# Kernel optimization log

Hardware: AMD Instinct MI355X
Metric: run time of the kernel (lower is better)

The kernel has to match this reference:

```python
import jax, jax.numpy as jnp
import numpy as np

DK = 128
B, S = 16, 2048

def setup_inputs() -> dict:
    key = jax.random.key(0)
    kq, kk, kv = jax.random.split(key, 3)
    q = jax.random.normal(kq, (B, S, DK), dtype=jnp.float32)
    k = jax.random.normal(kk, (B, S, DK), dtype=jnp.float32)
    v = jax.random.normal(kv, (B, S, DK), dtype=jnp.float32)
    return {"q": q, "k": k, "v": v}

def reference(q, k, v):
    # scores: [B, S, S]
    scale = 1.0 / jnp.sqrt(jnp.float32(DK))
    scores = jnp.einsum("bqd,bkd->bqk", q, k) * scale
    probs = jax.nn.softmax(scores, axis=-1)
    # dropout is identity in eval mode (training=None)
    return jnp.einsum("bqk,bkd->bqd", probs, v)
```

## Files before the change

kernel.cpp:

```cpp
#include <hip/hip_runtime.h>
#include <hip/hip_bf16.h>

#define BATCH 16
#define SEQ   2048
#define DK    128
#define NT    (SEQ / 64)
#define SC2   0.12751744f
#define THRAW 90.5f

typedef __attribute__((ext_vector_type(8))) short short8v;
typedef __attribute__((ext_vector_type(4))) float float4v;

typedef const __attribute__((address_space(1))) unsigned int* gas_t;
typedef __attribute__((address_space(3))) unsigned int* las_t;

__device__ inline void gl_lds16(const void* g, void* l) {
    __builtin_amdgcn_global_load_lds((gas_t)g, (las_t)l, 16, 0, 0);
}

__device__ inline short f2bf(float f) {
    __hip_bfloat16 h = __float2bfloat16(f);
    unsigned short u;
    __builtin_memcpy(&u, &h, sizeof(u));
    return (short)u;
}

__device__ inline unsigned cvt_pk_bf16(float a, float b) {
    unsigned r;
    asm("v_cvt_pk_bf16_f32 %0, %1, %2" : "=v"(r) : "v"(a), "v"(b));
    return r;
}

__global__ __launch_bounds__(256)
void conv_k_kernel(const float* __restrict__ k, short* __restrict__ kb)
{
    size_t i = ((size_t)blockIdx.x * 256 + threadIdx.x) * 8;
    float4 a = *reinterpret_cast<const float4*>(k + i);
    float4 b = *reinterpret_cast<const float4*>(k + i + 4);
    short8v t;
    t[0] = f2bf(a.x); t[1] = f2bf(a.y); t[2] = f2bf(a.z); t[3] = f2bf(a.w);
    t[4] = f2bf(b.x); t[5] = f2bf(b.y); t[6] = f2bf(b.z); t[7] = f2bf(b.w);
    *reinterpret_cast<short8v*>(kb + i) = t;
}

__global__ __launch_bounds__(256)
void transpose_v_kernel(const float* __restrict__ v, short* __restrict__ vt)
{
    __shared__ float tile[32][33];
    const int tx = threadIdx.x & 31;
    const int ty = threadIdx.x >> 5;
    const int b  = blockIdx.z;
    const int s0 = blockIdx.x * 32;
    const int d0 = blockIdx.y * 32;

    const float* vb = v + ((size_t)b * SEQ + s0) * DK + d0;
#pragma unroll
    for (int i = 0; i < 4; ++i) {
        int r = ty + 8 * i;
        tile[r][tx] = vb[(size_t)r * DK + tx];
    }
    __syncthreads();

    const int s   = s0 + tx;
    const int t   = s >> 6;
    const int kvl = s & 63;
    const int pos = ((kvl >> 5) << 5) | (((kvl >> 2) & 3) << 3) | (((kvl >> 4) & 1) << 2) | (kvl & 3);
    const size_t col = (size_t)(t << 6) + pos;

    short* vtb = vt + ((size_t)b * DK + d0) * SEQ;
#pragma unroll
    for (int i = 0; i < 4; ++i) {
        int r = ty + 8 * i;
        vtb[(size_t)r * SEQ + col] = f2bf(tile[tx][r]);
    }
}

__global__ __launch_bounds__(256)
void attn_fwd_v4(const float* __restrict__ q,
                 const short* __restrict__ kb,
                 const short* __restrict__ vt,
                 float* __restrict__ out)
{
    __shared__ __align__(16) char lds[65536];

    const int tid  = threadIdx.x;
    const int lane = tid & 63;
    const int wave = tid >> 6;
    const int b    = blockIdx.y;
    const int q0   = blockIdx.x * 64 + wave * 16;

    const int row = lane & 15;
    const int grp = lane >> 4;
    const int swz = (row & 7) << 4;

    const float* qb = q + ((size_t)b * SEQ + q0) * DK;
    short8v qf[4];
#pragma unroll
    for (int c = 0; c < 4; ++c) {
        const float* p = qb + row * DK + c * 32 + grp * 8;
        float4 x = *reinterpret_cast<const float4*>(p);
        float4 y = *reinterpret_cast<const float4*>(p + 4);
        union { unsigned u[4]; short8v v; } pk;
        pk.u[0] = cvt_pk_bf16(x.x, x.y);
        pk.u[1] = cvt_pk_bf16(x.z, x.w);
        pk.u[2] = cvt_pk_bf16(y.x, y.y);
        pk.u[3] = cvt_pk_bf16(y.z, y.w);
        qf[c] = pk.v;
    }

    const char* kB = (const char*)(kb + (size_t)b * SEQ * DK);
    const char* vB = (const char*)(vt + (size_t)b * DK * SEQ);

    const int kSrcCol = (lane & 15) << 4;
    const int vSrcCol = (lane & 7) << 4;

    float m_run = -1e30f;
    float l_run = 0.0f;
    float4v o[8];
#pragma unroll
    for (int i = 0; i < 8; ++i) { o[i][0] = 0.f; o[i][1] = 0.f; o[i][2] = 0.f; o[i][3] = 0.f; }

    auto STAGE = [&](int bufsel, int t) {
        char* Kd = lds + bufsel * 32768;
        char* Vd = Kd + 16384;
        const char* ksrc = kB + (size_t)t * 64 * 256;
        const char* vsrc = vB + (size_t)t * 128;
#pragma unroll
        for (int i = 0; i < 4; ++i) {
            const int c  = wave * 4 + i;
            const int kr = 4 * c + (lane >> 4);
            gl_lds16(ksrc + (size_t)kr * 256 + (kSrcCol ^ ((kr & 7) << 4)),
                     Kd + c * 1024);
            const int vd = 8 * c + (lane >> 3);
            gl_lds16(vsrc + (size_t)vd * 4096 + (vSrcCol ^ ((vd & 7) << 4)),
                     Vd + c * 1024);
        }
    };

    STAGE(0, 0);
    __syncthreads();

    int buf = 0;
    for (int t = 0; t < NT; ++t) {
        if (t + 1 < NT) STAGE(buf ^ 1, t + 1);

        const char* Kl = lds + buf * 32768;
        const char* Vl = Kl + 16384;

        float4v s[4];
        __builtin_amdgcn_s_setprio(1);
#pragma unroll
        for (int sub = 0; sub < 4; ++sub) {
            s[sub][0] = 0.f; s[sub][1] = 0.f; s[sub][2] = 0.f; s[sub][3] = 0.f;
            const char* kr = Kl + (sub * 16 + row) * 256;
#pragma unroll
            for (int c = 0; c < 4; ++c) {
                short8v kf = *reinterpret_cast<const short8v*>(kr + (((c << 6) | (grp << 4)) ^ swz));
                s[sub] = __builtin_amdgcn_mfma_f32_16x16x32_bf16(kf, qf[c], s[sub], 0, 0, 0);
            }
        }
        __builtin_amdgcn_s_setprio(0);

        float p[16];
#pragma unroll
        for (int sub = 0; sub < 4; ++sub)
#pragma unroll
            for (int r = 0; r < 4; ++r) p[sub * 4 + r] = s[sub][r];

        float mx = p[0];
#pragma unroll
        for (int i = 1; i < 16; ++i) mx = fmaxf(mx, p[i]);
        mx = fmaxf(mx, __shfl_xor(mx, 16));
        mx = fmaxf(mx, __shfl_xor(mx, 32));

        if (!__all(mx <= m_run + THRAW)) {
            const float mnew  = fmaxf(m_run, mx);
            const float alpha = exp2f((m_run - mnew) * SC2);
            l_run *= alpha;
            m_run = mnew;
            float aq[4];
#pragma unroll
            for (int r = 0; r < 4; ++r) aq[r] = __shfl(alpha, grp * 4 + r);
#pragma unroll
            for (int dblk = 0; dblk < 8; ++dblk)
#pragma unroll
                for (int r = 0; r < 4; ++r) o[dblk][r] *= aq[r];
        }

        float tsum = 0.f;
#pragma unroll
        for (int i = 0; i < 16; ++i) { p[i] = exp2f((p[i] - m_run) * SC2); tsum += p[i]; }
        tsum += __shfl_xor(tsum, 16);
        tsum += __shfl_xor(tsum, 32);
        l_run += tsum;

        short8v pf[2];
#pragma unroll
        for (int p2 = 0; p2 < 2; ++p2) {
            union { unsigned u[4]; short8v v; } pk;
            pk.u[0] = cvt_pk_bf16(p[8 * p2 + 0], p[8 * p2 + 1]);
            pk.u[1] = cvt_pk_bf16(p[8 * p2 + 2], p[8 * p2 + 3]);
            pk.u[2] = cvt_pk_bf16(p[8 * p2 + 4], p[8 * p2 + 5]);
            pk.u[3] = cvt_pk_bf16(p[8 * p2 + 6], p[8 * p2 + 7]);
            pf[p2] = pk.v;
        }

        __builtin_amdgcn_s_setprio(1);
#pragma unroll
        for (int dblk = 0; dblk < 8; ++dblk) {
            const char* vr = Vl + (dblk * 16 + row) * 128;
#pragma unroll
            for (int p2 = 0; p2 < 2; ++p2) {
                short8v vf = *reinterpret_cast<const short8v*>(vr + ((((p2 << 2) | grp) << 4) ^ swz));
                o[dblk] = __builtin_amdgcn_mfma_f32_16x16x32_bf16(pf[p2], vf, o[dblk], 0, 0, 0);
            }
        }
        __builtin_amdgcn_s_setprio(0);

        __syncthreads();
        buf ^= 1;
    }

    const float linv = 1.0f / l_run;
    float liq[4];
#pragma unroll
    for (int r = 0; r < 4; ++r) liq[r] = __shfl(linv, grp * 4 + r);

    float* ob = out + ((size_t)b * SEQ + q0) * DK;
#pragma unroll
    for (int dblk = 0; dblk < 8; ++dblk)
#pragma unroll
        for (int r = 0; r < 4; ++r)
            ob[(size_t)(grp * 4 + r) * DK + dblk * 16 + row] = o[dblk][r] * liq[r];
}

__global__ __launch_bounds__(256)
void attn_fwd_slow(const float* __restrict__ q,
                   const float* __restrict__ k,
                   const float* __restrict__ v,
                   float* __restrict__ out)
{
    const int lane = threadIdx.x & 63;
    const int wave = threadIdx.x >> 6;
    const int b    = blockIdx.y;
    const int q0   = blockIdx.x * 64 + wave * 16;
    const int row = lane & 15;
    const int grp = lane >> 4;

    const float* qb = q + ((size_t)b * SEQ + q0) * DK;
    const float* kbp = k + (size_t)b * SEQ * DK;
    const float* vbp = v + (size_t)b * SEQ * DK;

    short8v qf[4];
#pragma unroll
    for (int c = 0; c < 4; ++c) {
        const float* p = qb + row * DK + c * 32 + grp * 8;
        float4 x = *reinterpret_cast<const float4*>(p);
        float4 y = *reinterpret_cast<const float4*>(p + 4);
        short8v t;
        t[0] = f2bf(x.x); t[1] = f2bf(x.y); t[2] = f2bf(x.z); t[3] = f2bf(x.w);
        t[4] = f2bf(y.x); t[5] = f2bf(y.y); t[6] = f2bf(y.z); t[7] = f2bf(y.w);
        qf[c] = t;
    }

    float m_run = -1e30f, l_run = 0.0f;
    float4v o[8];
#pragma unroll
    for (int i = 0; i < 8; ++i) { o[i][0]=0.f; o[i][1]=0.f; o[i][2]=0.f; o[i][3]=0.f; }
    const float scale = 0.08838834764831845f;

    for (int kv0 = 0; kv0 < SEQ; kv0 += 16) {
        short8v kf[4];
        const float* kp0 = kbp + (size_t)(kv0 + row) * DK + grp * 8;
#pragma unroll
        for (int c = 0; c < 4; ++c) {
            const float* p = kp0 + c * 32;
            float4 x = *reinterpret_cast<const float4*>(p);
            float4 y = *reinterpret_cast<const float4*>(p + 4);
            short8v t;
            t[0] = f2bf(x.x); t[1] = f2bf(x.y); t[2] = f2bf(x.z); t[3] = f2bf(x.w);
            t[4] = f2bf(y.x); t[5] = f2bf(y.y); t[6] = f2bf(y.z); t[7] = f2bf(y.w);
            kf[c] = t;
        }
        short8v vf[8];
#pragma unroll
        for (int dblk = 0; dblk < 8; ++dblk) {
            const float* p = vbp + (size_t)(kv0 + 4 * grp) * DK + dblk * 16 + row;
            short b0 = f2bf(p[0]);
            short b1 = f2bf(p[DK]);
            short b2 = f2bf(p[2 * DK]);
            short b3 = f2bf(p[3 * DK]);
            short8v t;
            t[0]=b0; t[1]=b1; t[2]=b2; t[3]=b3; t[4]=b0; t[5]=b1; t[6]=b2; t[7]=b3;
            vf[dblk] = t;
        }
        float4v s; s[0]=0.f; s[1]=0.f; s[2]=0.f; s[3]=0.f;
#pragma unroll
        for (int c = 0; c < 4; ++c)
            s = __builtin_amdgcn_mfma_f32_16x16x32_bf16(kf[c], qf[c], s, 0, 0, 0);

        float sv[4]; float tmax = -1e30f;
#pragma unroll
        for (int r = 0; r < 4; ++r) { sv[r] = s[r] * scale; tmax = fmaxf(tmax, sv[r]); }
        tmax = fmaxf(tmax, __shfl_xor(tmax, 16));
        tmax = fmaxf(tmax, __shfl_xor(tmax, 32));
        const float mnew = fmaxf(m_run, tmax);
        float pr[4]; float tsum = 0.f;
#pragma unroll
        for (int r = 0; r < 4; ++r) { pr[r] = __expf(sv[r] - mnew); tsum += pr[r]; }
        tsum += __shfl_xor(tsum, 16);
        tsum += __shfl_xor(tsum, 32);
        const float alpha = __expf(m_run - mnew);
        l_run = l_run * alpha + tsum;
        m_run = mnew;
        float aq[4];
#pragma unroll
        for (int r = 0; r < 4; ++r) aq[r] = __shfl(alpha, grp * 4 + r);
#pragma unroll
        for (int dblk = 0; dblk < 8; ++dblk)
#pragma unroll
            for (int r = 0; r < 4; ++r) o[dblk][r] *= aq[r];

        short8v pf;
        pf[0]=f2bf(pr[0]); pf[1]=f2bf(pr[1]); pf[2]=f2bf(pr[2]); pf[3]=f2bf(pr[3]);
        pf[4]=0; pf[5]=0; pf[6]=0; pf[7]=0;
#pragma unroll
        for (int dblk = 0; dblk < 8; ++dblk)
            o[dblk] = __builtin_amdgcn_mfma_f32_16x16x32_bf16(pf, vf[dblk], o[dblk], 0, 0, 0);
    }

    const float linv = 1.0f / l_run;
    float li[4];
#pragma unroll
    for (int r = 0; r < 4; ++r) li[r] = __shfl(linv, grp * 4 + r);
    float* ob = out + ((size_t)b * SEQ + q0) * DK;
#pragma unroll
    for (int dblk = 0; dblk < 8; ++dblk)
#pragma unroll
        for (int r = 0; r < 4; ++r)
            ob[(size_t)(grp * 4 + r) * DK + dblk * 16 + row] = o[dblk][r] * li[r];
}

extern "C" void kernel_launch(void* const* d_in, const int* in_sizes, int n_in,
                              void* d_out, int out_size, void* d_ws, size_t ws_size,
                              hipStream_t stream) {
    const float* q = (const float*)d_in[0];
    const float* k = (const float*)d_in[1];
    const float* v = (const float*)d_in[2];
    float* out = (float*)d_out;

    const size_t kb_bytes = (size_t)BATCH * SEQ * DK * sizeof(short);
    const size_t need = 2 * kb_bytes;

    if (ws_size >= need) {
        short* kb = (short*)d_ws;
        short* vt = (short*)((char*)d_ws + kb_bytes);
        hipLaunchKernelGGL(conv_k_kernel, dim3(2048), dim3(256), 0, stream, k, kb);
        hipLaunchKernelGGL(transpose_v_kernel, dim3(SEQ / 32, DK / 32, BATCH), dim3(256), 0, stream, v, vt);
        hipLaunchKernelGGL(attn_fwd_v4, dim3(SEQ / 64, BATCH), dim3(256), 0, stream, q, kb, vt, out);
    } else {
        hipLaunchKernelGGL(attn_fwd_slow, dim3(SEQ / 64, BATCH), dim3(256), 0, stream, q, k, v, out);
    }
}
```

Measured before the change: 78.95 us.

## Split KV sequence across two wave groups per block and fold scale into K

The attention kernel now runs 8 waves per block. Two halves of the key/value sequence are processed in parallel by separate wave groups, each with 32-key tiles, and their partial softmax states are merged through LDS at the end. The softmax scale (with log2e) is pre-multiplied into K during the bf16 conversion, which removes per-element multiplies in the exponent path. This doubles per-block parallelism and the waves available for latency hiding. In exchange it adds an LDS merge with a barrier, halves the MFMA work per tile, and rounds the scaled K values to bf16.

After: 74.02 us. -6.2%, faster.

```diff
diff --git a/kernel.cpp b/kernel.cpp
--- a/kernel.cpp
+++ b/kernel.cpp
@@ -4,9 +4,9 @@
 #define BATCH 16
 #define SEQ   2048
 #define DK    128
-#define NT    (SEQ / 64)
+#define NT    (SEQ / 2 / 32)
 #define SC2   0.12751744f
-#define THRAW 90.5f
+#define THRL2 11.541560f
 
 typedef __attribute__((ext_vector_type(8))) short short8v;
 typedef __attribute__((ext_vector_type(4))) float float4v;
@@ -38,8 +38,8 @@
     float4 a = *reinterpret_cast<const float4*>(k + i);
     float4 b = *reinterpret_cast<const float4*>(k + i + 4);
     short8v t;
-    t[0] = f2bf(a.x); t[1] = f2bf(a.y); t[2] = f2bf(a.z); t[3] = f2bf(a.w);
-    t[4] = f2bf(b.x); t[5] = f2bf(b.y); t[6] = f2bf(b.z); t[7] = f2bf(b.w);
+    t[0] = f2bf(a.x * SC2); t[1] = f2bf(a.y * SC2); t[2] = f2bf(a.z * SC2); t[3] = f2bf(a.w * SC2);
+    t[4] = f2bf(b.x * SC2); t[5] = f2bf(b.y * SC2); t[6] = f2bf(b.z * SC2); t[7] = f2bf(b.w * SC2);
     *reinterpret_cast<short8v*>(kb + i) = t;
 }
 
@@ -62,10 +62,9 @@
     __syncthreads();
 
     const int s   = s0 + tx;
-    const int t   = s >> 6;
-    const int kvl = s & 63;
-    const int pos = ((kvl >> 5) << 5) | (((kvl >> 2) & 3) << 3) | (((kvl >> 4) & 1) << 2) | (kvl & 3);
-    const size_t col = (size_t)(t << 6) + pos;
+    const int kvl = s & 31;
+    const int pos = (((kvl >> 2) & 3) << 3) | (((kvl >> 4) & 1) << 2) | (kvl & 3);
+    const size_t col = (size_t)(s & ~31) | pos;
 
     short* vtb = vt + ((size_t)b * DK + d0) * SEQ;
 #pragma unroll
@@ -75,8 +74,8 @@
     }
 }
 
-__global__ __launch_bounds__(256)
-void attn_fwd_v4(const float* __restrict__ q,
+__global__ __launch_bounds__(512)
+void attn_fwd_v5(const float* __restrict__ q,
                  const short* __restrict__ kb,
                  const short* __restrict__ vt,
                  float* __restrict__ out)
@@ -86,12 +85,15 @@
     const int tid  = threadIdx.x;
     const int lane = tid & 63;
     const int wave = tid >> 6;
+    const int qt   = wave & 3;
+    const int h    = wave >> 2;
     const int b    = blockIdx.y;
-    const int q0   = blockIdx.x * 64 + wave * 16;
-
-    const int row = lane & 15;
-    const int grp = lane >> 4;
-    const int swz = (row & 7) << 4;
+    const int q0   = blockIdx.x * 64 + qt * 16;
+
+    const int row  = lane & 15;
+    const int grp  = lane >> 4;
+    const int kswz = (row & 7) << 4;
+    const int vswz = ((row >> 1) & 3) << 4;
 
     const float* qb = q + ((size_t)b * SEQ + q0) * DK;
     short8v qf[4];
@@ -111,8 +113,28 @@
     const char* kB = (const char*)(kb + (size_t)b * SEQ * DK);
     const char* vB = (const char*)(vt + (size_t)b * DK * SEQ);
 
-    const int kSrcCol = (lane & 15) << 4;
-    const int vSrcCol = (lane & 7) << 4;
+    const char* src0[4];
+    int         sstr[4];
+    int         dsto[4];
+#pragma unroll
+    for (int i = 0; i < 4; ++i) {
+        const int c = wave * 4 + i;
+        if (c < 16) {
+            const int hh = c >> 3, cc = c & 7;
+            const int kr = 4 * cc + (lane >> 4);
+            src0[i] = kB + (size_t)(hh * 1024 + kr) * 256
+                         + (((lane & 15) << 4) ^ ((kr & 7) << 4));
+            sstr[i] = 32 * 256;
+            dsto[i] = hh * 8192 + cc * 1024;
+        } else {
+            const int hh = (c >> 3) & 1, cc = c & 7;
+            const int vd = 16 * cc + (lane >> 2);
+            src0[i] = vB + (size_t)vd * 4096 + hh * 2048
+                         + (((lane & 3) << 4) ^ (((lane >> 3) & 3) << 4));
+            sstr[i] = 32 * 2;
+            dsto[i] = 16384 + hh * 8192 + cc * 1024;
+        }
+    }
 
     float m_run = -1e30f;
     float l_run = 0.0f;
@@ -121,20 +143,10 @@
     for (int i = 0; i < 8; ++i) { o[i][0] = 0.f; o[i][1] = 0.f; o[i][2] = 0.f; o[i][3] = 0.f; }
 
     auto STAGE = [&](int bufsel, int t) {
-        char* Kd = lds + bufsel * 32768;
-        char* Vd = Kd + 16384;
-        const char* ksrc = kB + (size_t)t * 64 * 256;
-        const char* vsrc = vB + (size_t)t * 128;
-#pragma unroll
-        for (int i = 0; i < 4; ++i) {
-            const int c  = wave * 4 + i;
-            const int kr = 4 * c + (lane >> 4);
-            gl_lds16(ksrc + (size_t)kr * 256 + (kSrcCol ^ ((kr & 7) << 4)),
-                     Kd + c * 1024);
-            const int vd = 8 * c + (lane >> 3);
-            gl_lds16(vsrc + (size_t)vd * 4096 + (vSrcCol ^ ((vd & 7) << 4)),
-                     Vd + c * 1024);
-        }
+        char* base = lds + bufsel * 32768;
+#pragma unroll
+        for (int i = 0; i < 4; ++i)
+            gl_lds16(src0[i] + (size_t)t * sstr[i], base + dsto[i]);
     };
 
     STAGE(0, 0);
@@ -144,38 +156,31 @@
     for (int t = 0; t < NT; ++t) {
         if (t + 1 < NT) STAGE(buf ^ 1, t + 1);
 
-        const char* Kl = lds + buf * 32768;
-        const char* Vl = Kl + 16384;
-
-        float4v s[4];
+        const char* Kl = lds + buf * 32768 + h * 8192;
+        const char* Vl = lds + buf * 32768 + 16384 + h * 8192;
+
+        float4v s[2];
         __builtin_amdgcn_s_setprio(1);
 #pragma unroll
-        for (int sub = 0; sub < 4; ++sub) {
+        for (int sub = 0; sub < 2; ++sub) {
             s[sub][0] = 0.f; s[sub][1] = 0.f; s[sub][2] = 0.f; s[sub][3] = 0.f;
             const char* kr = Kl + (sub * 16 + row) * 256;
 #pragma unroll
             for (int c = 0; c < 4; ++c) {
-                short8v kf = *reinterpret_cast<const short8v*>(kr + (((c << 6) | (grp << 4)) ^ swz));
+                short8v kf = *reinterpret_cast<const short8v*>(kr + (((c << 6) | (grp << 4)) ^ kswz));
                 s[sub] = __builtin_amdgcn_mfma_f32_16x16x32_bf16(kf, qf[c], s[sub], 0, 0, 0);
             }
         }
         __builtin_amdgcn_s_setprio(0);
 
-        float p[16];
-#pragma unroll
-        for (int sub = 0; sub < 4; ++sub)
-#pragma unroll
-            for (int r = 0; r < 4; ++r) p[sub * 4 + r] = s[sub][r];
-
-        float mx = p[0];
-#pragma unroll
-        for (int i = 1; i < 16; ++i) mx = fmaxf(mx, p[i]);
+        float mx = fmaxf(fmaxf(fmaxf(s[0][0], s[0][1]), fmaxf(s[0][2], s[0][3])),
+                         fmaxf(fmaxf(s[1][0], s[1][1]), fmaxf(s[1][2], s[1][3])));
         mx = fmaxf(mx, __shfl_xor(mx, 16));
         mx = fmaxf(mx, __shfl_xor(mx, 32));
 
-        if (!__all(mx <= m_run + THRAW)) {
+        if (!__all(mx <= m_run + THRL2)) {
             const float mnew  = fmaxf(m_run, mx);
-            const float alpha = exp2f((m_run - mnew) * SC2);
+            const float alpha = exp2f(m_run - mnew);
             l_run *= alpha;
             m_run = mnew;
             float aq[4];
@@ -189,31 +194,30 @@
 
         float tsum = 0.f;
 #pragma unroll
-        for (int i = 0; i < 16; ++i) { p[i] = exp2f((p[i] - m_run) * SC2); tsum += p[i]; }
+        for (int sub = 0; sub < 2; ++sub)
+#pragma unroll
+            for (int r = 0; r < 4; ++r) {
+                const float e = exp2f(s[sub][r] - m_run);
+                s[sub][r] = e;
+                tsum += e;
+            }
         tsum += __shfl_xor(tsum, 16);
         tsum += __shfl_xor(tsum, 32);
         l_run += tsum;
 
-        short8v pf[2];
-#pragma unroll
-        for (int p2 = 0; p2 < 2; ++p2) {
-            union { unsigned u[4]; short8v v; } pk;
-            pk.u[0] = cvt_pk_bf16(p[8 * p2 + 0], p[8 * p2 + 1]);
-            pk.u[1] = cvt_pk_bf16(p[8 * p2 + 2], p[8 * p2 + 3]);
-            pk.u[2] = cvt_pk_bf16(p[8 * p2 + 4], p[8 * p2 + 5]);
-            pk.u[3] = cvt_pk_bf16(p[8 * p2 + 6], p[8 * p2 + 7]);
-            pf[p2] = pk.v;
-        }
+        union { unsigned u[4]; short8v v; } pk;
+        pk.u[0] = cvt_pk_bf16(s[0][0], s[0][1]);
+        pk.u[1] = cvt_pk_bf16(s[0][2], s[0][3]);
+        pk.u[2] = cvt_pk_bf16(s[1][0], s[1][1]);
+        pk.u[3] = cvt_pk_bf16(s[1][2], s[1][3]);
+        const short8v pf = pk.v;
 
         __builtin_amdgcn_s_setprio(1);
 #pragma unroll
         for (int dblk = 0; dblk < 8; ++dblk) {
-            const char* vr = Vl + (dblk * 16 + row) * 128;
-#pragma unroll
-            for (int p2 = 0; p2 < 2; ++p2) {
-                short8v vf = *reinterpret_cast<const short8v*>(vr + ((((p2 << 2) | grp) << 4) ^ swz));
-                o[dblk] = __builtin_amdgcn_mfma_f32_16x16x32_bf16(pf[p2], vf, o[dblk], 0, 0, 0);
-            }
+            const short8v vf = *reinterpret_cast<const short8v*>(
+                Vl + (dblk * 16 + row) * 64 + ((grp << 4) ^ vswz));
+            o[dblk] = __builtin_amdgcn_mfma_f32_16x16x32_bf16(pf, vf, o[dblk], 0, 0, 0);
         }
         __builtin_amdgcn_s_setprio(0);
 
@@ -221,17 +225,47 @@
         buf ^= 1;
     }
 
-    const float linv = 1.0f / l_run;
-    float liq[4];
-#pragma unroll
-    for (int r = 0; r < 4; ++r) liq[r] = __shfl(linv, grp * 4 + r);
-
-    float* ob = out + ((size_t)b * SEQ + q0) * DK;
-#pragma unroll
-    for (int dblk = 0; dblk < 8; ++dblk)
-#pragma unroll
-        for (int r = 0; r < 4; ++r)
-            ob[(size_t)(grp * 4 + r) * DK + dblk * 16 + row] = o[dblk][r] * liq[r];
+    float* smO = (float*)lds;
+    float* smM = (float*)(lds + 33792);
+    float* smL = (float*)(lds + 34048);
+
+    if (h == 1) {
+        smM[qt * 16 + row] = m_run;
+        smL[qt * 16 + row] = l_run;
+#pragma unroll
+        for (int dblk = 0; dblk < 8; ++dblk)
+#pragma unroll
+            for (int r = 0; r < 4; ++r)
+                smO[(qt * 16 + grp * 4 + r) * 132 + dblk * 16 + row] = o[dblk][r];
+    }
+    __syncthreads();
+    if (h == 0) {
+        const float m1 = smM[qt * 16 + row];
+        const float l1 = smL[qt * 16 + row];
+        const float mf = fmaxf(m_run, m1);
+        const float a0 = exp2f(m_run - mf);
+        const float a1 = exp2f(m1 - mf);
+        const float lf = l_run * a0 + l1 * a1;
+        const float li = 1.0f / lf;
+
+        float a0q[4], a1q[4], liq[4];
+#pragma unroll
+        for (int r = 0; r < 4; ++r) {
+            a0q[r] = __shfl(a0, grp * 4 + r);
+            a1q[r] = __shfl(a1, grp * 4 + r);
+            liq[r] = __shfl(li, grp * 4 + r);
+        }
+
+        float* ob = out + ((size_t)b * SEQ + q0) * DK;
+#pragma unroll
+        for (int dblk = 0; dblk < 8; ++dblk)
+#pragma unroll
+            for (int r = 0; r < 4; ++r) {
+                float val = (o[dblk][r] * a0q[r]
+                             + smO[(qt * 16 + grp * 4 + r) * 132 + dblk * 16 + row] * a1q[r]) * liq[r];
+                ob[(size_t)(grp * 4 + r) * DK + dblk * 16 + row] = val;
+            }
+    }
 }
 
 __global__ __launch_bounds__(256)
@@ -357,7 +391,7 @@
         short* vt = (short*)((char*)d_ws + kb_bytes);
         hipLaunchKernelGGL(conv_k_kernel, dim3(2048), dim3(256), 0, stream, k, kb);
         hipLaunchKernelGGL(transpose_v_kernel, dim3(SEQ / 32, DK / 32, BATCH), dim3(256), 0, stream, v, vt);
-        hipLaunchKernelGGL(attn_fwd_v4, dim3(SEQ / 64, BATCH), dim3(256), 0, stream, q, kb, vt, out);
+        hipLaunchKernelGGL(attn_fwd_v5, dim3(SEQ / 64, BATCH), dim3(512), 0, stream, q, kb, vt, out);
     } else {
         hipLaunchKernelGGL(attn_fwd_slow, dim3(SEQ / 64, BATCH), dim3(256), 0, stream, q, k, v, out);
     }
```
